# Kernel optimization log

Measured on AMD Instinct MI355X. Metric: run time of the kernel, lower is better.

The kernel has to match this reference:

```python
import jax, jax.numpy as jnp
import numpy as np

V, E, H, B, T = 50000, 300, 150, 64, 512  # vocab, embed_dim, hidden_dim, batch, seq_len
ATTN = H // 2


def setup_inputs() -> dict:
    key = jax.random.key(0)
    ks = jax.random.split(key, 18)
    s = 0.08
    inp = {
        "texts": jax.random.randint(ks[0], (B, T), 0, V, dtype=jnp.int32),
        "lengths": jax.random.randint(ks[1], (B,), 1, T + 1, dtype=jnp.int32),
        "emb_table": jax.random.normal(ks[2], (V, E), jnp.float32) * s,
        # layer 0 GRU (torch gate order: reset | update | new)
        "Wih0": jax.random.normal(ks[3], (3 * H, E), jnp.float32) * s,
        "Whh0": jax.random.normal(ks[4], (3 * H, H), jnp.float32) * s,
        "bih0": jax.random.normal(ks[5], (3 * H,), jnp.float32) * s,
        "bhh0": jax.random.normal(ks[6], (3 * H,), jnp.float32) * s,
        # layer 1 GRU
        "Wih1": jax.random.normal(ks[7], (3 * H, H), jnp.float32) * s,
        "Whh1": jax.random.normal(ks[8], (3 * H, H), jnp.float32) * s,
        "bih1": jax.random.normal(ks[9], (3 * H,), jnp.float32) * s,
        "bhh1": jax.random.normal(ks[10], (3 * H,), jnp.float32) * s,
        # additive attention
        "W1": jax.random.normal(ks[11], (ATTN, H), jnp.float32) * s,
        "w2": jax.random.normal(ks[12], (1, ATTN), jnp.float32) * s,
        # classifier head
        "fc1_w": jax.random.normal(ks[13], (H, H), jnp.float32) * s,
        "fc1_b": jax.random.normal(ks[14], (H,), jnp.float32) * s,
        "fc2_w": jax.random.normal(ks[15], (1, H), jnp.float32) * s,
        "fc2_b": jax.random.normal(ks[16], (1,), jnp.float32) * s,
    }
    return inp


def _gru_layer(x, Wih, Whh, bih, bhh, mask):
    # x: [T, B, I]; mask: [T, B, 1] True where t < length (packed-sequence semantics)
    h0 = jnp.zeros((x.shape[1], Whh.shape[1]), x.dtype)
    xw = x @ Wih.T + bih  # precompute input projections for all steps: [T, B, 3H]

    def step(h, inp):
        xw_t, m = inp
        hg = h @ Whh.T + bhh
        xr, xz, xn = jnp.split(xw_t, 3, axis=-1)
        hr, hz, hn = jnp.split(hg, 3, axis=-1)
        r = jax.nn.sigmoid(xr + hr)
        z = jax.nn.sigmoid(xz + hz)
        n = jnp.tanh(xn + r * hn)
        h_new = (1.0 - z) * n + z * h
        h_next = jnp.where(m, h_new, h)        # hidden freezes past length
        out = jnp.where(m, h_new, 0.0)          # pad_packed_sequence pads with zeros
        return h_next, out

    h_last, outs = jax.lax.scan(step, h0, (xw, mask))
    return outs, h_last


def reference(texts, lengths, emb_table, Wih0, Whh0, bih0, bhh0,
              Wih1, Whh1, bih1, bhh1, W1, w2, fc1_w, fc1_b, fc2_w, fc2_b):
    emb = emb_table[texts]                    # [B, T, E]
    x = jnp.transpose(emb, (1, 0, 2))         # [T, B, E] (batch_first=False)
    t_idx = jnp.arange(x.shape[0], dtype=lengths.dtype)
    mask = (t_idx[:, None] < lengths[None, :])[:, :, None]  # [T, B, 1]

    out0, _ = _gru_layer(x, Wih0, Whh0, bih0, bhh0, mask)
    out1, _ = _gru_layer(out0, Wih1, Whh1, bih1, bhh1, mask)  # [T, B, H]

    # additive attention over time (unmasked softmax, matching the original)
    scores = (jnp.tanh(out1 @ W1.T) @ w2.T)[..., 0].T        # [B, T]
    attn = jax.nn.softmax(scores, axis=1)                    # [B, T]
    ctx = jnp.einsum('bt,tbh->bh', attn, out1)               # [B, H]

    hcls = jax.nn.relu(ctx @ fc1_w.T + fc1_b)
    logits = (hcls @ fc2_w.T + fc2_b)[:, 0]                  # [B]
    return logits
```

## Files before the change

### kernel.cpp

```cpp
#include <hip/hip_runtime.h>

#define TT 512
#define BB 64
#define EE 300
#define HH 150
#define G3 450
#define AT 75

typedef float v2f __attribute__((ext_vector_type(2)));

__device__ __forceinline__ float fast_rcp(float x) { return __builtin_amdgcn_rcpf(x); }
__device__ __forceinline__ float sigmoid_f(float x) { return fast_rcp(1.f + __expf(-x)); }
__device__ __forceinline__ float tanh_f(float x) {
  float e = __expf(2.f * x);
  return 1.f - 2.f * fast_rcp(e + 1.f);
}

__global__ void k_prep(const float* __restrict__ Wih0, const float* __restrict__ Whh0,
                       const float* __restrict__ Wih1, const float* __restrict__ Whh1,
                       const float* __restrict__ W1,   const float* __restrict__ fc1w,
                       float* __restrict__ Wih0T, float* __restrict__ Whh0T,
                       float* __restrict__ Wih1T, float* __restrict__ Whh1T,
                       float* __restrict__ W1T,   float* __restrict__ fc1T) {
  int tid = blockIdx.x * blockDim.x + threadIdx.x;
  int nt = gridDim.x * blockDim.x;
  for (int i = tid; i < G3 * EE; i += nt) { int r = i / EE, c = i - r * EE; Wih0T[c * G3 + r] = Wih0[i]; }
  for (int i = tid; i < G3 * HH; i += nt) { int r = i / HH, c = i - r * HH; Whh0T[c * G3 + r] = Whh0[i]; }
  for (int i = tid; i < G3 * HH; i += nt) { int r = i / HH, c = i - r * HH; Wih1T[c * G3 + r] = Wih1[i]; }
  for (int i = tid; i < G3 * HH; i += nt) { int r = i / HH, c = i - r * HH; Whh1T[c * G3 + r] = Whh1[i]; }
  for (int i = tid; i < AT * HH; i += nt) { int r = i / HH, c = i - r * HH; W1T[c * AT + r] = W1[i]; }
  for (int i = tid; i < HH * HH; i += nt) { int r = i / HH, c = i - r * HH; fc1T[c * HH + r] = fc1w[i]; }
}

__global__ __launch_bounds__(512) void k_xw0(const int* __restrict__ texts,
                                             const float* __restrict__ emb,
                                             const float* __restrict__ WihT,
                                             const float* __restrict__ bih,
                                             float* __restrict__ xw) {
  __shared__ __align__(16) float a_lds[32 * EE];
  const int row0 = blockIdx.x * 32;
  const int tid = threadIdx.x;
  for (int p = tid; p < 32 * EE; p += 512) {
    int r = p / EE, e = p - r * EE;
    int vrow = texts[row0 + r];
    a_lds[p] = emb[(size_t)vrow * EE + e];
  }
  __syncthreads();
  const int g = tid;
  if (g < G3) {
    float acc[32];
#pragma unroll
    for (int r = 0; r < 32; ++r) acc[r] = 0.f;
    const float bias = bih[g];
    for (int k = 0; k < EE; k += 4) {
      float w0 = WihT[(k + 0) * G3 + g];
      float w1 = WihT[(k + 1) * G3 + g];
      float w2v = WihT[(k + 2) * G3 + g];
      float w3 = WihT[(k + 3) * G3 + g];
#pragma unroll
      for (int r = 0; r < 32; ++r) {
        const float4 av = *reinterpret_cast<const float4*>(&a_lds[r * EE + k]);
        acc[r] = fmaf(av.x, w0, acc[r]);
        acc[r] = fmaf(av.y, w1, acc[r]);
        acc[r] = fmaf(av.z, w2v, acc[r]);
        acc[r] = fmaf(av.w, w3, acc[r]);
      }
    }
#pragma unroll
    for (int r = 0; r < 32; ++r) xw[(size_t)(row0 + r) * G3 + g] = acc[r] + bias;
  }
}

__global__ __launch_bounds__(512) void k_xw1(const float* __restrict__ in,
                                             const float* __restrict__ WihT,
                                             const float* __restrict__ bih,
                                             float* __restrict__ xw) {
  __shared__ __align__(16) float a_lds[32 * 152];
  const int row0 = blockIdx.x * 32;
  const int tid = threadIdx.x;
  for (int p = tid; p < 32 * HH; p += 512) {
    int r = p / HH, e = p - r * HH;
    a_lds[r * 152 + e] = in[(size_t)(row0 + r) * HH + e];
  }
  __syncthreads();
  const int g = tid;
  if (g < G3) {
    float acc[32];
#pragma unroll
    for (int r = 0; r < 32; ++r) acc[r] = 0.f;
    const float bias = bih[g];
    for (int k = 0; k < 148; k += 4) {
      float w0 = WihT[(k + 0) * G3 + g];
      float w1 = WihT[(k + 1) * G3 + g];
      float w2v = WihT[(k + 2) * G3 + g];
      float w3 = WihT[(k + 3) * G3 + g];
#pragma unroll
      for (int r = 0; r < 32; ++r) {
        const float4 av = *reinterpret_cast<const float4*>(&a_lds[r * 152 + k]);
        acc[r] = fmaf(av.x, w0, acc[r]);
        acc[r] = fmaf(av.y, w1, acc[r]);
        acc[r] = fmaf(av.z, w2v, acc[r]);
        acc[r] = fmaf(av.w, w3, acc[r]);
      }
    }
    {
      float w0 = WihT[148 * G3 + g];
      float w1 = WihT[149 * G3 + g];
#pragma unroll
      for (int r = 0; r < 32; ++r) {
        acc[r] = fmaf(a_lds[r * 152 + 148], w0, acc[r]);
        acc[r] = fmaf(a_lds[r * 152 + 149], w1, acc[r]);
      }
    }
#pragma unroll
    for (int r = 0; r < 32; ++r) xw[(size_t)(row0 + r) * G3 + g] = acc[r] + bias;
  }
}

__global__ __launch_bounds__(512, 2) void k_rec(const float* __restrict__ WhhT,
                                                const float* __restrict__ bhh,
                                                const float* __restrict__ xw,
                                                const int* __restrict__ lengths,
                                                float* __restrict__ out) {
  const int b = blockIdx.x;
  const int tid = threadIdx.x;
  __shared__ __align__(16) float h_lds[152];
  __shared__ float hg_lds[G3];
  const int len = lengths[b];

  const bool active = tid < G3;
  const int g = active ? tid : 0;

  v2f w[75];
#pragma unroll
  for (int k = 0; k < 75; ++k) {
    w[k][0] = WhhT[(2 * k) * G3 + g];
    w[k][1] = WhhT[(2 * k + 1) * G3 + g];
  }
#pragma unroll
  for (int k = 0; k < 75; ++k) asm volatile("" : "+v"(w[k]));

  const float bias = bhh[g];
  if (tid < 152) h_lds[tid] = 0.f;
  float h_reg = 0.f;
  __syncthreads();

  const float* xwb = xw + (size_t)b * TT * G3;
  float* outb = out + (size_t)b * TT * HH;
  const float4* h4 = reinterpret_cast<const float4*>(h_lds);

  for (int t = 0; t < len; ++t) {
    float xr = 0.f, xz = 0.f, xn = 0.f;
    if (tid < HH) {
      const float* xwt = xwb + (size_t)t * G3;
      xr = xwt[tid]; xz = xwt[tid + HH]; xn = xwt[tid + 2 * HH];
    }
    v2f a0 = {0.f, 0.f}, a1 = {0.f, 0.f};
#pragma unroll
    for (int q = 0; q < 37; ++q) {
      const float4 hv = h4[q];
      v2f hx = {hv.x, hv.y};
      v2f hy = {hv.z, hv.w};
      a0 = __builtin_elementwise_fma(w[2 * q], hx, a0);
      a1 = __builtin_elementwise_fma(w[2 * q + 1], hy, a1);
    }
    {
      const float4 hv = h4[37];
      v2f hx = {hv.x, hv.y};
      a0 = __builtin_elementwise_fma(w[74], hx, a0);
    }
    if (active) hg_lds[g] = bias + (a0[0] + a1[0]) + (a0[1] + a1[1]);
    __syncthreads();

    if (tid < HH) {
      const float hr = hg_lds[tid], hz = hg_lds[tid + HH], hn = hg_lds[tid + 2 * HH];
      const float r = sigmoid_f(xr + hr);
      const float z = sigmoid_f(xz + hz);
      const float n = tanh_f(xn + r * hn);
      const float hnew = (1.f - z) * n + z * h_reg;
      h_reg = hnew;
      h_lds[tid] = hnew;
      outb[(size_t)t * HH + tid] = hnew;
    }
    __syncthreads();
  }
  const int rem = (TT - len) * HH;
  float* outp = outb + (size_t)len * HH;
  for (int p = tid; p < rem; p += 512) outp[p] = 0.f;
}

__global__ __launch_bounds__(256) void k_scores(const float* __restrict__ out1,
                                                const float* __restrict__ W1T,
                                                const float* __restrict__ w2,
                                                float* __restrict__ scores) {
  const int row0 = blockIdx.x * 32;
  const int tid = threadIdx.x;
  __shared__ float sc[32];
  if (tid < 32) sc[tid] = 0.f;
  __syncthreads();
  for (int p = tid; p < 32 * AT; p += 256) {
    const int r = p / AT, a = p - r * AT;
    const float* x = out1 + (size_t)(row0 + r) * HH;
    float a0 = 0.f, a1 = 0.f;
    for (int k = 0; k < HH; k += 2) {
      a0 = fmaf(W1T[k * AT + a], x[k], a0);
      a1 = fmaf(W1T[(k + 1) * AT + a], x[k + 1], a1);
    }
    atomicAdd(&sc[r], tanh_f(a0 + a1) * w2[a]);
  }
  __syncthreads();
  if (tid < 32) scores[row0 + tid] = sc[tid];
}

__global__ __launch_bounds__(512) void k_final(const float* __restrict__ out1,
                                               const float* __restrict__ scores,
                                               const float* __restrict__ fc1T,
                                               const float* __restrict__ fc1b,
                                               const float* __restrict__ fc2w,
                                               const float* __restrict__ fc2b,
                                               float* __restrict__ logits) {
  const int b = blockIdx.x;
  const int tid = threadIdx.x;
  __shared__ float attn[TT];
  __shared__ float red[16];
  __shared__ float ctx[152];
  __shared__ float h1[152];

  float s = scores[b * TT + tid];
  float m = s;
#pragma unroll
  for (int off = 32; off > 0; off >>= 1) m = fmaxf(m, __shfl_xor(m, off));
  const int wave = tid >> 6;
  if ((tid & 63) == 0) red[wave] = m;
  __syncthreads();
  if (tid == 0) {
    float mm = red[0];
#pragma unroll
    for (int i = 1; i < 8; ++i) mm = fmaxf(mm, red[i]);
    red[8] = mm;
  }
  __syncthreads();
  const float mx = red[8];
  const float e = __expf(s - mx);
  attn[tid] = e;
  float zz = e;
#pragma unroll
  for (int off = 32; off > 0; off >>= 1) zz += __shfl_xor(zz, off);
  if ((tid & 63) == 0) red[wave] = zz;
  __syncthreads();
  if (tid == 0) {
    float ss = 0.f;
#pragma unroll
    for (int i = 0; i < 8; ++i) ss += red[i];
    red[9] = ss;
  }
  __syncthreads();
  const float invZ = 1.f / red[9];

  if (tid < HH) {
    const float* o1b = out1 + (size_t)b * TT * HH;
    float c0 = 0.f, c1 = 0.f, c2 = 0.f, c3 = 0.f;
    for (int t = 0; t < TT; t += 4) {
      c0 = fmaf(attn[t + 0], o1b[(t + 0) * HH + tid], c0);
      c1 = fmaf(attn[t + 1], o1b[(t + 1) * HH + tid], c1);
      c2 = fmaf(attn[t + 2], o1b[(t + 2) * HH + tid], c2);
      c3 = fmaf(attn[t + 3], o1b[(t + 3) * HH + tid], c3);
    }
    ctx[tid] = ((c0 + c1) + (c2 + c3)) * invZ;
  }
  __syncthreads();
  if (tid < HH) {
    float d0 = 0.f, d1 = 0.f;
    for (int k = 0; k < HH; k += 2) {
      d0 = fmaf(fc1T[k * HH + tid], ctx[k], d0);
      d1 = fmaf(fc1T[(k + 1) * HH + tid], ctx[k + 1], d1);
    }
    h1[tid] = fmaxf(d0 + d1 + fc1b[tid], 0.f);
  }
  __syncthreads();
  if (tid == 0) {
    float acc = fc2b[0];
    for (int k = 0; k < HH; ++k) acc = fmaf(fc2w[k], h1[k], acc);
    logits[b] = acc;
  }
}

extern "C" void kernel_launch(void* const* d_in, const int* in_sizes, int n_in,
                              void* d_out, int out_size, void* d_ws, size_t ws_size,
                              hipStream_t stream) {
  const int* texts     = (const int*)d_in[0];
  const int* lengths   = (const int*)d_in[1];
  const float* emb     = (const float*)d_in[2];
  const float* Wih0    = (const float*)d_in[3];
  const float* Whh0    = (const float*)d_in[4];
  const float* bih0    = (const float*)d_in[5];
  const float* bhh0    = (const float*)d_in[6];
  const float* Wih1    = (const float*)d_in[7];
  const float* Whh1    = (const float*)d_in[8];
  const float* bih1    = (const float*)d_in[9];
  const float* bhh1    = (const float*)d_in[10];
  const float* W1      = (const float*)d_in[11];
  const float* w2      = (const float*)d_in[12];
  const float* fc1w    = (const float*)d_in[13];
  const float* fc1b    = (const float*)d_in[14];
  const float* fc2w    = (const float*)d_in[15];
  const float* fc2b    = (const float*)d_in[16];
  float* logits = (float*)d_out;

  float* ws = (float*)d_ws;
  size_t off = 0;
  auto alloc = [&](size_t n) { float* p = ws + off; off += (n + 3) & ~(size_t)3; return p; };
  float* Wih0T  = alloc((size_t)G3 * EE);
  float* Whh0T  = alloc((size_t)G3 * HH);
  float* Wih1T  = alloc((size_t)G3 * HH);
  float* Whh1T  = alloc((size_t)G3 * HH);
  float* W1T    = alloc((size_t)AT * HH);
  float* fc1T   = alloc((size_t)HH * HH);
  float* xwbuf  = alloc((size_t)BB * TT * G3);
  float* out0   = alloc((size_t)BB * TT * HH);
  float* out1   = alloc((size_t)BB * TT * HH);
  float* scores = alloc((size_t)BB * TT);
  (void)ws_size; (void)in_sizes; (void)n_in; (void)out_size;

  hipLaunchKernelGGL(k_prep, dim3(256), dim3(256), 0, stream,
                     Wih0, Whh0, Wih1, Whh1, W1, fc1w,
                     Wih0T, Whh0T, Wih1T, Whh1T, W1T, fc1T);
  hipLaunchKernelGGL(k_xw0, dim3((BB * TT) / 32), dim3(512), 0, stream, texts, emb, Wih0T, bih0, xwbuf);
  hipLaunchKernelGGL(k_rec, dim3(BB), dim3(512), 0, stream, Whh0T, bhh0, xwbuf, lengths, out0);
  hipLaunchKernelGGL(k_xw1, dim3((BB * TT) / 32), dim3(512), 0, stream, out0, Wih1T, bih1, xwbuf);
  hipLaunchKernelGGL(k_rec, dim3(BB), dim3(512), 0, stream, Whh1T, bhh1, xwbuf, lengths, out1);
  hipLaunchKernelGGL(k_scores, dim3((BB * TT) / 32), dim3(256), 0, stream, out1, W1T, w2, scores);
  hipLaunchKernelGGL(k_final, dim3(BB), dim3(512), 0, stream, out1, scores, fc1T, fc1b, fc2w, fc2b, logits);
}
```

Baseline: 1.291 ms.

## Split GRU recurrence over K halves with readlane broadcasts; retile input projections

The recurrent kernel now has each thread own two gate rows and half of the hidden dimension, with weights pre-packed by a new k_pack kernel. Hidden-state values are broadcast through readlane into scalar registers and fed to packed FMAs. The two halves' partial sums are combined through LDS, which adds one extra barrier per step. The input-projection GEMMs now use 128-thread blocks, each thread computing four gate columns for register reuse, and layer 1 pads its K dimension to 152 with zeros to drop the tail loop.

```diff
diff --git a/kernel.cpp b/kernel.cpp
--- a/kernel.cpp
+++ b/kernel.cpp
@@ -16,167 +16,211 @@
   return 1.f - 2.f * fast_rcp(e + 1.f);
 }
 
-__global__ void k_prep(const float* __restrict__ Wih0, const float* __restrict__ Whh0,
-                       const float* __restrict__ Wih1, const float* __restrict__ Whh1,
+__global__ void k_prep(const float* __restrict__ Wih0, const float* __restrict__ Wih1,
                        const float* __restrict__ W1,   const float* __restrict__ fc1w,
-                       float* __restrict__ Wih0T, float* __restrict__ Whh0T,
-                       float* __restrict__ Wih1T, float* __restrict__ Whh1T,
+                       float* __restrict__ Wih0T, float* __restrict__ Wih1Tp,
                        float* __restrict__ W1T,   float* __restrict__ fc1T) {
   int tid = blockIdx.x * blockDim.x + threadIdx.x;
   int nt = gridDim.x * blockDim.x;
   for (int i = tid; i < G3 * EE; i += nt) { int r = i / EE, c = i - r * EE; Wih0T[c * G3 + r] = Wih0[i]; }
-  for (int i = tid; i < G3 * HH; i += nt) { int r = i / HH, c = i - r * HH; Whh0T[c * G3 + r] = Whh0[i]; }
-  for (int i = tid; i < G3 * HH; i += nt) { int r = i / HH, c = i - r * HH; Wih1T[c * G3 + r] = Wih1[i]; }
-  for (int i = tid; i < G3 * HH; i += nt) { int r = i / HH, c = i - r * HH; Whh1T[c * G3 + r] = Whh1[i]; }
+  for (int i = tid; i < 152 * G3; i += nt) {
+    int k = i / G3, g = i - k * G3;
+    Wih1Tp[i] = (k < HH) ? Wih1[g * HH + k] : 0.f;
+  }
   for (int i = tid; i < AT * HH; i += nt) { int r = i / HH, c = i - r * HH; W1T[c * AT + r] = W1[i]; }
   for (int i = tid; i < HH * HH; i += nt) { int r = i / HH, c = i - r * HH; fc1T[c * HH + r] = fc1w[i]; }
 }
 
-__global__ __launch_bounds__(512) void k_xw0(const int* __restrict__ texts,
-                                             const float* __restrict__ emb,
-                                             const float* __restrict__ WihT,
-                                             const float* __restrict__ bih,
-                                             float* __restrict__ xw) {
+__global__ void k_pack(const float* __restrict__ Whh, float* __restrict__ Wpk) {
+  int f = blockIdx.x * 256 + threadIdx.x;
+  if (f >= 512 * 152) return;
+  int tid = f / 152, o = f - tid * 152;
+  int s = tid >> 8, p = tid & 255;
+  int q = o >> 2, c = o & 3, r = c >> 1, half = c & 1;
+  int row = 2 * p + r, k = 74 * s + 2 * q + half;
+  float v = 0.f;
+  if (p < 225) {
+    bool dead = (s == 0 && k >= 75) || (s == 1 && k < 75);
+    if (!dead) v = Whh[row * HH + k];
+  }
+  Wpk[f] = v;
+}
+
+__global__ __launch_bounds__(128, 2) void k_xw0(const int* __restrict__ texts,
+                                                const float* __restrict__ emb,
+                                                const float* __restrict__ WihT,
+                                                const float* __restrict__ bih,
+                                                float* __restrict__ xw) {
   __shared__ __align__(16) float a_lds[32 * EE];
   const int row0 = blockIdx.x * 32;
   const int tid = threadIdx.x;
-  for (int p = tid; p < 32 * EE; p += 512) {
+  for (int p = tid; p < 32 * EE; p += 128) {
     int r = p / EE, e = p - r * EE;
-    int vrow = texts[row0 + r];
-    a_lds[p] = emb[(size_t)vrow * EE + e];
-  }
-  __syncthreads();
-  const int g = tid;
-  if (g < G3) {
-    float acc[32];
-#pragma unroll
-    for (int r = 0; r < 32; ++r) acc[r] = 0.f;
-    const float bias = bih[g];
-    for (int k = 0; k < EE; k += 4) {
-      float w0 = WihT[(k + 0) * G3 + g];
-      float w1 = WihT[(k + 1) * G3 + g];
-      float w2v = WihT[(k + 2) * G3 + g];
-      float w3 = WihT[(k + 3) * G3 + g];
-#pragma unroll
-      for (int r = 0; r < 32; ++r) {
-        const float4 av = *reinterpret_cast<const float4*>(&a_lds[r * EE + k]);
-        acc[r] = fmaf(av.x, w0, acc[r]);
-        acc[r] = fmaf(av.y, w1, acc[r]);
-        acc[r] = fmaf(av.z, w2v, acc[r]);
-        acc[r] = fmaf(av.w, w3, acc[r]);
-      }
-    }
-#pragma unroll
-    for (int r = 0; r < 32; ++r) xw[(size_t)(row0 + r) * G3 + g] = acc[r] + bias;
-  }
-}
-
-__global__ __launch_bounds__(512) void k_xw1(const float* __restrict__ in,
-                                             const float* __restrict__ WihT,
-                                             const float* __restrict__ bih,
-                                             float* __restrict__ xw) {
+    a_lds[p] = emb[(size_t)texts[row0 + r] * EE + e];
+  }
+  __syncthreads();
+  const int g0 = tid, g1 = tid + 128, g2 = tid + 256;
+  const bool has3 = (tid + 384) < G3;
+  const int g3 = has3 ? tid + 384 : 0;
+  float acc0[32], acc1[32], acc2[32], acc3[32];
+#pragma unroll
+  for (int r = 0; r < 32; ++r) { acc0[r] = 0.f; acc1[r] = 0.f; acc2[r] = 0.f; acc3[r] = 0.f; }
+  const float4* a4 = reinterpret_cast<const float4*>(a_lds);
+  for (int k = 0; k < EE; k += 4) {
+    float wA[4], wB[4], wC[4], wD[4];
+#pragma unroll
+    for (int i = 0; i < 4; ++i) {
+      const float* wr = WihT + (size_t)(k + i) * G3;
+      wA[i] = wr[g0]; wB[i] = wr[g1]; wC[i] = wr[g2]; wD[i] = wr[g3];
+    }
+#pragma unroll
+    for (int r = 0; r < 32; ++r) {
+      const float4 av = a4[r * 75 + (k >> 2)];
+      acc0[r] = fmaf(av.x, wA[0], acc0[r]); acc0[r] = fmaf(av.y, wA[1], acc0[r]);
+      acc0[r] = fmaf(av.z, wA[2], acc0[r]); acc0[r] = fmaf(av.w, wA[3], acc0[r]);
+      acc1[r] = fmaf(av.x, wB[0], acc1[r]); acc1[r] = fmaf(av.y, wB[1], acc1[r]);
+      acc1[r] = fmaf(av.z, wB[2], acc1[r]); acc1[r] = fmaf(av.w, wB[3], acc1[r]);
+      acc2[r] = fmaf(av.x, wC[0], acc2[r]); acc2[r] = fmaf(av.y, wC[1], acc2[r]);
+      acc2[r] = fmaf(av.z, wC[2], acc2[r]); acc2[r] = fmaf(av.w, wC[3], acc2[r]);
+      acc3[r] = fmaf(av.x, wD[0], acc3[r]); acc3[r] = fmaf(av.y, wD[1], acc3[r]);
+      acc3[r] = fmaf(av.z, wD[2], acc3[r]); acc3[r] = fmaf(av.w, wD[3], acc3[r]);
+    }
+  }
+  const float b0 = bih[g0], b1 = bih[g1], b2 = bih[g2], b3 = bih[g3];
+#pragma unroll
+  for (int r = 0; r < 32; ++r) {
+    float* o = xw + (size_t)(row0 + r) * G3;
+    o[g0] = acc0[r] + b0; o[g1] = acc1[r] + b1; o[g2] = acc2[r] + b2;
+    if (has3) o[g3] = acc3[r] + b3;
+  }
+}
+
+__global__ __launch_bounds__(128, 2) void k_xw1(const float* __restrict__ in,
+                                                const float* __restrict__ WihTp,
+                                                const float* __restrict__ bih,
+                                                float* __restrict__ xw) {
   __shared__ __align__(16) float a_lds[32 * 152];
   const int row0 = blockIdx.x * 32;
   const int tid = threadIdx.x;
-  for (int p = tid; p < 32 * HH; p += 512) {
-    int r = p / HH, e = p - r * HH;
-    a_lds[r * 152 + e] = in[(size_t)(row0 + r) * HH + e];
-  }
-  __syncthreads();
-  const int g = tid;
-  if (g < G3) {
-    float acc[32];
-#pragma unroll
-    for (int r = 0; r < 32; ++r) acc[r] = 0.f;
-    const float bias = bih[g];
-    for (int k = 0; k < 148; k += 4) {
-      float w0 = WihT[(k + 0) * G3 + g];
-      float w1 = WihT[(k + 1) * G3 + g];
-      float w2v = WihT[(k + 2) * G3 + g];
-      float w3 = WihT[(k + 3) * G3 + g];
-#pragma unroll
-      for (int r = 0; r < 32; ++r) {
-        const float4 av = *reinterpret_cast<const float4*>(&a_lds[r * 152 + k]);
-        acc[r] = fmaf(av.x, w0, acc[r]);
-        acc[r] = fmaf(av.y, w1, acc[r]);
-        acc[r] = fmaf(av.z, w2v, acc[r]);
-        acc[r] = fmaf(av.w, w3, acc[r]);
-      }
-    }
-    {
-      float w0 = WihT[148 * G3 + g];
-      float w1 = WihT[149 * G3 + g];
-#pragma unroll
-      for (int r = 0; r < 32; ++r) {
-        acc[r] = fmaf(a_lds[r * 152 + 148], w0, acc[r]);
-        acc[r] = fmaf(a_lds[r * 152 + 149], w1, acc[r]);
-      }
-    }
-#pragma unroll
-    for (int r = 0; r < 32; ++r) xw[(size_t)(row0 + r) * G3 + g] = acc[r] + bias;
-  }
-}
-
-__global__ __launch_bounds__(512, 2) void k_rec(const float* __restrict__ WhhT,
+  for (int p = tid; p < 32 * 152; p += 128) {
+    int r = p / 152, e = p - r * 152;
+    a_lds[p] = (e < HH) ? in[(size_t)(row0 + r) * HH + e] : 0.f;
+  }
+  __syncthreads();
+  const int g0 = tid, g1 = tid + 128, g2 = tid + 256;
+  const bool has3 = (tid + 384) < G3;
+  const int g3 = has3 ? tid + 384 : 0;
+  float acc0[32], acc1[32], acc2[32], acc3[32];
+#pragma unroll
+  for (int r = 0; r < 32; ++r) { acc0[r] = 0.f; acc1[r] = 0.f; acc2[r] = 0.f; acc3[r] = 0.f; }
+  const float4* a4 = reinterpret_cast<const float4*>(a_lds);
+  for (int k = 0; k < 152; k += 4) {
+    float wA[4], wB[4], wC[4], wD[4];
+#pragma unroll
+    for (int i = 0; i < 4; ++i) {
+      const float* wr = WihTp + (size_t)(k + i) * G3;
+      wA[i] = wr[g0]; wB[i] = wr[g1]; wC[i] = wr[g2]; wD[i] = wr[g3];
+    }
+#pragma unroll
+    for (int r = 0; r < 32; ++r) {
+      const float4 av = a4[r * 38 + (k >> 2)];
+      acc0[r] = fmaf(av.x, wA[0], acc0[r]); acc0[r] = fmaf(av.y, wA[1], acc0[r]);
+      acc0[r] = fmaf(av.z, wA[2], acc0[r]); acc0[r] = fmaf(av.w, wA[3], acc0[r]);
+      acc1[r] = fmaf(av.x, wB[0], acc1[r]); acc1[r] = fmaf(av.y, wB[1], acc1[r]);
+      acc1[r] = fmaf(av.z, wB[2], acc1[r]); acc1[r] = fmaf(av.w, wB[3], acc1[r]);
+      acc2[r] = fmaf(av.x, wC[0], acc2[r]); acc2[r] = fmaf(av.y, wC[1], acc2[r]);
+      acc2[r] = fmaf(av.z, wC[2], acc2[r]); acc2[r] = fmaf(av.w, wC[3], acc2[r]);
+      acc3[r] = fmaf(av.x, wD[0], acc3[r]); acc3[r] = fmaf(av.y, wD[1], acc3[r]);
+      acc3[r] = fmaf(av.z, wD[2], acc3[r]); acc3[r] = fmaf(av.w, wD[3], acc3[r]);
+    }
+  }
+  const float b0 = bih[g0], b1 = bih[g1], b2 = bih[g2], b3 = bih[g3];
+#pragma unroll
+  for (int r = 0; r < 32; ++r) {
+    float* o = xw + (size_t)(row0 + r) * G3;
+    o[g0] = acc0[r] + b0; o[g1] = acc1[r] + b1; o[g2] = acc2[r] + b2;
+    if (has3) o[g3] = acc3[r] + b3;
+  }
+}
+
+__global__ __launch_bounds__(512, 2) void k_rec(const float* __restrict__ Wpk,
                                                 const float* __restrict__ bhh,
                                                 const float* __restrict__ xw,
                                                 const int* __restrict__ lengths,
                                                 float* __restrict__ out) {
   const int b = blockIdx.x;
   const int tid = threadIdx.x;
-  __shared__ __align__(16) float h_lds[152];
-  __shared__ float hg_lds[G3];
+  const int lane = tid & 63;
+  __shared__ float h_lds[160];
+  __shared__ float part[452];
+  __shared__ float hg[452];
   const int len = lengths[b];
 
-  const bool active = tid < G3;
-  const int g = active ? tid : 0;
-
-  v2f w[75];
-#pragma unroll
-  for (int k = 0; k < 75; ++k) {
-    w[k][0] = WhhT[(2 * k) * G3 + g];
-    w[k][1] = WhhT[(2 * k + 1) * G3 + g];
-  }
-#pragma unroll
-  for (int k = 0; k < 75; ++k) asm volatile("" : "+v"(w[k]));
-
-  const float bias = bhh[g];
-  if (tid < 152) h_lds[tid] = 0.f;
+  const int s = tid >> 8;
+  const int p = tid & 255;
+  const bool act = p < 225;
+  const int base = s * 74;
+
+  v2f w0[38], w1[38];
+  {
+    const float4* wp = reinterpret_cast<const float4*>(Wpk + (size_t)tid * 152);
+#pragma unroll
+    for (int q = 0; q < 38; ++q) {
+      const float4 f = wp[q];
+      w0[q][0] = f.x; w0[q][1] = f.y;
+      w1[q][0] = f.z; w1[q][1] = f.w;
+    }
+  }
+  float2 bb = {0.f, 0.f};
+  if (act) bb = *reinterpret_cast<const float2*>(bhh + 2 * p);
+
+  for (int i = tid; i < 160; i += 512) h_lds[i] = 0.f;
   float h_reg = 0.f;
   __syncthreads();
 
   const float* xwb = xw + (size_t)b * TT * G3;
   float* outb = out + (size_t)b * TT * HH;
-  const float4* h4 = reinterpret_cast<const float4*>(h_lds);
 
   for (int t = 0; t < len; ++t) {
+#pragma unroll
+    for (int q = 0; q < 38; ++q) asm volatile("" : "+v"(w0[q]), "+v"(w1[q]));
     float xr = 0.f, xz = 0.f, xn = 0.f;
     if (tid < HH) {
       const float* xwt = xwb + (size_t)t * G3;
       xr = xwt[tid]; xz = xwt[tid + HH]; xn = xwt[tid + 2 * HH];
     }
+    const int i0 = __float_as_int(h_lds[base + lane]);
+    const int i1 = __float_as_int(h_lds[base + 64 + (lane & 15)]);
     v2f a0 = {0.f, 0.f}, a1 = {0.f, 0.f};
 #pragma unroll
-    for (int q = 0; q < 37; ++q) {
-      const float4 hv = h4[q];
-      v2f hx = {hv.x, hv.y};
-      v2f hy = {hv.z, hv.w};
-      a0 = __builtin_elementwise_fma(w[2 * q], hx, a0);
-      a1 = __builtin_elementwise_fma(w[2 * q + 1], hy, a1);
-    }
-    {
-      const float4 hv = h4[37];
-      v2f hx = {hv.x, hv.y};
-      a0 = __builtin_elementwise_fma(w[74], hx, a0);
-    }
-    if (active) hg_lds[g] = bias + (a0[0] + a1[0]) + (a0[1] + a1[1]);
+    for (int q = 0; q < 38; ++q) {
+      int lo, hi;
+      if (2 * q < 64) {
+        lo = __builtin_amdgcn_readlane(i0, 2 * q);
+        hi = __builtin_amdgcn_readlane(i0, 2 * q + 1);
+      } else {
+        lo = __builtin_amdgcn_readlane(i1, 2 * q - 64);
+        hi = __builtin_amdgcn_readlane(i1, 2 * q - 63);
+      }
+      const unsigned long long hp =
+          (unsigned long long)(unsigned)lo | ((unsigned long long)(unsigned)hi << 32);
+      asm("v_pk_fma_f32 %0, %1, %2, %0" : "+v"(a0) : "v"(w0[q]), "s"(hp));
+      asm("v_pk_fma_f32 %0, %1, %2, %0" : "+v"(a1) : "v"(w1[q]), "s"(hp));
+    }
+    const float pr0 = a0[0] + a0[1];
+    const float pr1 = a1[0] + a1[1];
+    if (s == 1 && act) *reinterpret_cast<float2*>(&part[2 * p]) = make_float2(pr0, pr1);
     __syncthreads();
-
+    if (s == 0 && act) {
+      const float2 pp = *reinterpret_cast<const float2*>(&part[2 * p]);
+      *reinterpret_cast<float2*>(&hg[2 * p]) =
+          make_float2(pr0 + pp.x + bb.x, pr1 + pp.y + bb.y);
+    }
+    __syncthreads();
     if (tid < HH) {
-      const float hr = hg_lds[tid], hz = hg_lds[tid + HH], hn = hg_lds[tid + 2 * HH];
-      const float r = sigmoid_f(xr + hr);
-      const float z = sigmoid_f(xz + hz);
-      const float n = tanh_f(xn + r * hn);
+      const float r = sigmoid_f(xr + hg[tid]);
+      const float z = sigmoid_f(xz + hg[tid + HH]);
+      const float n = tanh_f(xn + r * hg[tid + 2 * HH]);
       const float hnew = (1.f - z) * n + z * h_reg;
       h_reg = hnew;
       h_lds[tid] = hnew;
@@ -186,7 +230,7 @@
   }
   const int rem = (TT - len) * HH;
   float* outp = outb + (size_t)len * HH;
-  for (int p = tid; p < rem; p += 512) outp[p] = 0.f;
+  for (int i = tid; i < rem; i += 512) outp[i] = 0.f;
 }
 
 __global__ __launch_bounds__(256) void k_scores(const float* __restrict__ out1,
@@ -226,8 +270,8 @@
   __shared__ float ctx[152];
   __shared__ float h1[152];
 
-  float s = scores[b * TT + tid];
-  float m = s;
+  float sv = scores[b * TT + tid];
+  float m = sv;
 #pragma unroll
   for (int off = 32; off > 0; off >>= 1) m = fmaxf(m, __shfl_xor(m, off));
   const int wave = tid >> 6;
@@ -240,8 +284,7 @@
     red[8] = mm;
   }
   __syncthreads();
-  const float mx = red[8];
-  const float e = __expf(s - mx);
+  const float e = __expf(sv - red[8]);
   attn[tid] = e;
   float zz = e;
 #pragma unroll
@@ -311,11 +354,11 @@
   size_t off = 0;
   auto alloc = [&](size_t n) { float* p = ws + off; off += (n + 3) & ~(size_t)3; return p; };
   float* Wih0T  = alloc((size_t)G3 * EE);
-  float* Whh0T  = alloc((size_t)G3 * HH);
-  float* Wih1T  = alloc((size_t)G3 * HH);
-  float* Whh1T  = alloc((size_t)G3 * HH);
+  float* Wih1Tp = alloc((size_t)G3 * 152);
   float* W1T    = alloc((size_t)AT * HH);
   float* fc1T   = alloc((size_t)HH * HH);
+  float* Wpk0   = alloc((size_t)512 * 152);
+  float* Wpk1   = alloc((size_t)512 * 152);
   float* xwbuf  = alloc((size_t)BB * TT * G3);
   float* out0   = alloc((size_t)BB * TT * HH);
   float* out1   = alloc((size_t)BB * TT * HH);
@@ -323,12 +366,13 @@
   (void)ws_size; (void)in_sizes; (void)n_in; (void)out_size;
 
   hipLaunchKernelGGL(k_prep, dim3(256), dim3(256), 0, stream,
-                     Wih0, Whh0, Wih1, Whh1, W1, fc1w,
-                     Wih0T, Whh0T, Wih1T, Whh1T, W1T, fc1T);
-  hipLaunchKernelGGL(k_xw0, dim3((BB * TT) / 32), dim3(512), 0, stream, texts, emb, Wih0T, bih0, xwbuf);
-  hipLaunchKernelGGL(k_rec, dim3(BB), dim3(512), 0, stream, Whh0T, bhh0, xwbuf, lengths, out0);
-  hipLaunchKernelGGL(k_xw1, dim3((BB * TT) / 32), dim3(512), 0, stream, out0, Wih1T, bih1, xwbuf);
-  hipLaunchKernelGGL(k_rec, dim3(BB), dim3(512), 0, stream, Whh1T, bhh1, xwbuf, lengths, out1);
+                     Wih0, Wih1, W1, fc1w, Wih0T, Wih1Tp, W1T, fc1T);
+  hipLaunchKernelGGL(k_pack, dim3(304), dim3(256), 0, stream, Whh0, Wpk0);
+  hipLaunchKernelGGL(k_pack, dim3(304), dim3(256), 0, stream, Whh1, Wpk1);
+  hipLaunchKernelGGL(k_xw0, dim3((BB * TT) / 32), dim3(128), 0, stream, texts, emb, Wih0T, bih0, xwbuf);
+  hipLaunchKernelGGL(k_rec, dim3(BB), dim3(512), 0, stream, Wpk0, bhh0, xwbuf, lengths, out0);
+  hipLaunchKernelGGL(k_xw1, dim3((BB * TT) / 32), dim3(128), 0, stream, out0, Wih1Tp, bih1, xwbuf);
+  hipLaunchKernelGGL(k_rec, dim3(BB), dim3(512), 0, stream, Wpk1, bhh1, xwbuf, lengths, out1);
   hipLaunchKernelGGL(k_scores, dim3((BB * TT) / 32), dim3(256), 0, stream, out1, W1T, w2, scores);
   hipLaunchKernelGGL(k_final, dim3(BB), dim3(512), 0, stream, out1, scores, fc1T, fc1b, fc2w, fc2b, logits);
 }
```

New measurement: 1.346 ms. 1.04x slower.
